# Performance work log

Measured on AMD Instinct MI355X. Metric: run time of the kernel, lower is better.

The kernel has to match this reference:

```python
import jax, jax.numpy as jnp
import numpy as np

N_NODES = 100000
N_EDGES = 3200000
N_GRAPHS = 1000
FEAT = 512
EMB = 7
N_CLASSES = 10


def gcn_conv(x, W, b, src, dst, n_nodes):
    # PyG GCNConv: add self-loops, symmetric normalization, aggregate src->dst.
    h = x @ W  # [N, emb] — transform first (emb is tiny)
    loops = jnp.arange(n_nodes, dtype=src.dtype)
    es = jnp.concatenate([src, loops])
    ed = jnp.concatenate([dst, loops])
    deg = jax.ops.segment_sum(jnp.ones_like(ed, dtype=h.dtype), ed, num_segments=n_nodes)
    dinv = jnp.where(deg > 0, jax.lax.rsqrt(deg), 0.0)
    norm = dinv[es] * dinv[ed]  # [E+N]
    msgs = h[es] * norm[:, None]
    out = jax.ops.segment_sum(msgs, ed, num_segments=n_nodes)
    return out + b


def setup_inputs() -> dict:
    key = jax.random.key(0)
    ks = jax.random.split(key, 8)
    x = jax.random.normal(ks[0], (N_NODES, FEAT), dtype=jnp.float32)
    edge_index = jax.random.randint(ks[1], (2, N_EDGES), 0, N_NODES, dtype=jnp.int64)
    batch_index = jnp.sort(jax.random.randint(ks[2], (N_NODES,), 0, N_GRAPHS, dtype=jnp.int64))
    s_in = 1.0 / np.sqrt(FEAT)
    s_h = 1.0 / np.sqrt(EMB)
    W_in = jax.random.uniform(ks[3], (FEAT, EMB), jnp.float32, -s_in, s_in)
    b_in = jnp.zeros((EMB,), jnp.float32)
    W_conv1 = jax.random.uniform(ks[4], (EMB, EMB), jnp.float32, -s_h, s_h)
    b_conv1 = jnp.zeros((EMB,), jnp.float32)
    W_out = jax.random.uniform(ks[5], (EMB, N_CLASSES), jnp.float32, -s_h, s_h)
    b_out = jax.random.uniform(ks[6], (N_CLASSES,), jnp.float32, -s_h, s_h)
    return {"x": x, "edge_index": edge_index, "batch_index": batch_index,
            "W_in": W_in, "b_in": b_in, "W_conv1": W_conv1, "b_conv1": b_conv1,
            "W_out": W_out, "b_out": b_out}


def reference(x, edge_index, batch_index, W_in, b_in, W_conv1, b_conv1, W_out, b_out):
    src, dst = edge_index[0], edge_index[1]
    out = jax.nn.relu(gcn_conv(x, W_in, b_in, src, dst, N_NODES))  # [N, 7]
    # final_conv_acts (computed by the original but NOT used in the returned logits)
    _final_conv_acts = jax.nn.relu(gcn_conv(out, W_conv1, b_conv1, src, dst, N_NODES))
    # global mean pool over batch_index (on `out`, matching the original forward)
    sums = jax.ops.segment_sum(out, batch_index, num_segments=N_GRAPHS)
    counts = jax.ops.segment_sum(jnp.ones((N_NODES,), out.dtype), batch_index, num_segments=N_GRAPHS)
    pooled = sums / jnp.maximum(counts, 1.0)[:, None]  # [G, 7]
    logits = pooled @ W_out + b_out  # [G, classes]
    return jax.nn.softmax(logits, axis=1)
```

## Files before the change

### kernel.cpp

```cpp
#include <hip/hip_runtime.h>

#define N_NODES   100000
#define N_EDGES   3200000
#define N_GRAPHS  1000
#define FEAT      512
#define EMB       7
#define HP        8
#define N_CLASSES 10

#define BSH       8
#define DMASK     255
#define NBUCK     391
#define TCOLS     392
#define NB_A      512
#define TILE_A    6250
#define NIT       25
#define SEGCAP    9216
#define GSPAN     16
#define MMF       391

__device__ __forceinline__ int load_idx(const void* p, long long i, int is32) {
    if (is32) return ((const int*)p)[i];
    return (int)((const long long*)p)[i];
}

__device__ int edge_is32(const void* p) {
    __shared__ int sflag;
    if (threadIdx.x == 0) sflag = 0;
    __syncthreads();
    const int* w = (const int*)p;
    int any = 0;
    for (int k = threadIdx.x; k < 2048; k += blockDim.x)
        if (w[2 * k + 1] != 0) any = 1;
    if (any) atomicOr(&sflag, 1);
    __syncthreads();
    return sflag;
}

__device__ int batch_is32(const void* p) {
    __shared__ int sflag;
    if (threadIdx.x == 0) sflag = 0;
    __syncthreads();
    const int* w = (const int*)p;
    int any = 0;
    for (int k = 1024 + threadIdx.x; k < 2048; k += blockDim.x)
        if (w[2 * k + 1] != 0) any = 1;
    if (any) atomicOr(&sflag, 1);
    __syncthreads();
    return sflag;
}

__device__ void mm_span(int nbase, const float* __restrict__ x,
                        const float* __restrict__ W, float* __restrict__ h) {
    int n = nbase + (int)threadIdx.x;
    if (n >= N_NODES) return;
    const float4* xr = (const float4*)(x + (size_t)n * FEAT);
    float acc[EMB];
#pragma unroll
    for (int j = 0; j < EMB; ++j) acc[j] = 0.0f;
#pragma unroll 4
    for (int k4 = 0; k4 < FEAT / 4; ++k4) {
        float4 v = xr[k4];
        const float* w = W + k4 * 4 * EMB;
#pragma unroll
        for (int j = 0; j < EMB; ++j) {
            float a = acc[j];
            a = fmaf(v.x, w[0 * EMB + j], a);
            a = fmaf(v.y, w[1 * EMB + j], a);
            a = fmaf(v.z, w[2 * EMB + j], a);
            a = fmaf(v.w, w[3 * EMB + j], a);
            acc[j] = a;
        }
    }
    float4* o = (float4*)(h + (size_t)n * HP);
    o[0] = make_float4(acc[0], acc[1], acc[2], acc[3]);
    o[1] = make_float4(acc[4], acc[5], acc[6], 0.0f);
}

__global__ void k_sortblk(const void* __restrict__ eidx, int* __restrict__ T,
                          int* __restrict__ gpk, const float* __restrict__ x,
                          const float* __restrict__ W, float* __restrict__ h) {
    if (blockIdx.x >= NB_A) { mm_span(((int)blockIdx.x - NB_A) * 256, x, W, h); return; }
    __shared__ int stage[TILE_A];
    __shared__ int bins[NBUCK];
    __shared__ int cur[NBUCK];
    __shared__ int pairv[256];
    __shared__ int wsum[4];
    int is32 = edge_is32(eidx);
    const int b = (int)blockIdx.x, t = (int)threadIdx.x;
    for (int k = t; k < NBUCK; k += 256) bins[k] = 0;
    __syncthreads();
    long long e0 = (long long)b * TILE_A;
    int pk[NIT], bk[NIT];
#pragma unroll
    for (int it = 0; it < NIT; ++it) {
        int i = it * 256 + t;
        if (i < TILE_A) {
            int src = load_idx(eidx, e0 + i, is32);
            int d   = load_idx(eidx, (long long)N_EDGES + e0 + i, is32);
            pk[it] = src | ((d & DMASK) << 17);
            bk[it] = d >> BSH;
            atomicAdd(&bins[bk[it]], 1);
        } else { pk[it] = 0; bk[it] = -1; }
    }
    __syncthreads();
    int c0 = (2 * t     < NBUCK) ? bins[2 * t]     : 0;
    int c1 = (2 * t + 1 < NBUCK) ? bins[2 * t + 1] : 0;
    int pr = c0 + c1;
    int inc = pr;
    for (int o = 1; o < 64; o <<= 1) {
        int u = __shfl_up(inc, o);
        if ((t & 63) >= o) inc += u;
    }
    if ((t & 63) == 63) wsum[t >> 6] = inc;
    pairv[t] = inc;
    __syncthreads();
    int add = 0, wv = t >> 6;
    if (wv >= 1) add += wsum[0];
    if (wv >= 2) add += wsum[1];
    if (wv >= 3) add += wsum[2];
    int excl = inc + add - pr;
    __syncthreads();
    if (2 * t     < NBUCK) { bins[2 * t]     = excl;      cur[2 * t]     = excl; }
    if (2 * t + 1 < NBUCK) { bins[2 * t + 1] = excl + c0; cur[2 * t + 1] = excl + c0; }
    __syncthreads();
    for (int k = t; k < NBUCK; k += 256)
        T[b * TCOLS + k] = b * TILE_A + bins[k];
    if (t == 0) T[b * TCOLS + NBUCK] = (b + 1) * TILE_A;
#pragma unroll
    for (int it = 0; it < NIT; ++it) {
        if (bk[it] >= 0) {
            int slot = atomicAdd(&cur[bk[it]], 1);
            stage[slot] = pk[it];
        }
    }
    __syncthreads();
    for (int i = t; i < TILE_A; i += 256)
        gpk[b * TILE_A + i] = stage[i];
}

__device__ int load_runs(const int* __restrict__ T, int k,
                         int* rstart, int* rst, int* wsum) {
    const int t = (int)threadIdx.x;
    int b0 = 2 * t, b1 = 2 * t + 1;
    int s0 = T[b0 * TCOLS + k], e0 = T[b0 * TCOLS + k + 1];
    int s1 = T[b1 * TCOLS + k], e1 = T[b1 * TCOLS + k + 1];
    rstart[b0] = s0; rstart[b1] = s1;
    int c0 = e0 - s0, c1 = e1 - s1;
    int pr = c0 + c1;
    int inc = pr;
    for (int o = 1; o < 64; o <<= 1) {
        int u = __shfl_up(inc, o);
        if ((t & 63) >= o) inc += u;
    }
    if ((t & 63) == 63) wsum[t >> 6] = inc;
    __syncthreads();
    int add = 0, wv = t >> 6;
    if (wv >= 1) add += wsum[0];
    if (wv >= 2) add += wsum[1];
    if (wv >= 3) add += wsum[2];
    int excl = inc + add - pr;
    rst[b0] = excl;
    rst[b1] = excl + c0;
    if (t == 255) rst[512] = excl + pr;
    __syncthreads();
    return rst[512];
}

__device__ __forceinline__ int run_of(const int* rst, int i) {
    int lo = 0, hi = 512;
    while (lo + 1 < hi) { int m = (lo + hi) >> 1; if (rst[m] <= i) lo = m; else hi = m; }
    return lo;
}

__global__ void k_nodecnt(const int* __restrict__ T, const int* __restrict__ gpk,
                          int* __restrict__ cnt, float* __restrict__ gsum,
                          float* __restrict__ h) {
    __shared__ int rstart[512], rst[513], wsum[4];
    __shared__ int bin[256];
    const int k = (int)blockIdx.x, t = (int)threadIdx.x;
    if (k < 32) {
        int idx = k * 256 + t;
        if (idx < N_GRAPHS * 8) gsum[idx] = 0.0f;
    }
    bin[t] = 0;
    int total = load_runs(T, k, rstart, rst, wsum);
    __syncthreads();
    int chunk = (total + 255) >> 8;
    int i0 = t * chunk;
    int i1 = i0 + chunk; if (i1 > total) i1 = total;
    if (i0 < total) {
        int cur = run_of(rst, i0);
        int nxt = rst[cur + 1];
        int addr = rstart[cur] + (i0 - rst[cur]);
        for (int i = i0; i < i1; ++i) {
            while (i >= nxt) { ++cur; addr = rstart[cur] + (i - rst[cur]); nxt = rst[cur + 1]; }
            int p = gpk[addr++];
            atomicAdd(&bin[(p >> 17) & DMASK], 1);
        }
    }
    __syncthreads();
    int node = (k << BSH) + t;
    if (node < N_NODES) {
        int c = bin[t];
        cnt[node] = c;
        float di = rsqrtf((float)c + 1.0f);
        float4* hp = (float4*)(h + (size_t)node * HP);
        float4 a = hp[0], cc = hp[1];
        hp[0] = make_float4(a.x * di, a.y * di, a.z * di, a.w * di);
        hp[1] = make_float4(cc.x * di, cc.y * di, cc.z * di, 0.0f);
    }
}

__global__ void k_ggather(const int* __restrict__ T, const int* __restrict__ gpk,
                          const int* __restrict__ cnt, const float* __restrict__ h,
                          const float* __restrict__ b_in, const void* __restrict__ batch,
                          float* __restrict__ gsum) {
    __shared__ int stage[SEGCAP];
    __shared__ int rstart[512], rst[513], wsum[4];
    __shared__ int bin[256], loff[256], curs[256], pairv[256];
    __shared__ float gsl[GSPAN][8];
    __shared__ int gmin_s;
    const int k = (int)blockIdx.x, t = (int)threadIdx.x;
    int bis32 = batch_is32(batch);
    if (t == 0) gmin_s = load_idx(batch, (long long)(k << BSH), bis32);
    if (t < GSPAN * 8) ((float*)gsl)[t] = 0.0f;
    int total = load_runs(T, k, rstart, rst, wsum);
    int len = (total > SEGCAP) ? SEGCAP : total;
    {
        int node = (k << BSH) + t;
        bin[t] = (node < N_NODES) ? cnt[node] : 0;
        curs[t] = 0;
    }
    __syncthreads();
    const int gmin = gmin_s;
    {
        int v = bin[t];
        int inc = v;
        for (int o = 1; o < 64; o <<= 1) {
            int u = __shfl_up(inc, o);
            if ((t & 63) >= o) inc += u;
        }
        pairv[t] = inc;
        __syncthreads();
        int add = 0, wv = t >> 6;
        if (wv >= 1) add += pairv[63];
        if (wv >= 2) add += pairv[127];
        if (wv >= 3) add += pairv[191];
        loff[t] = inc + add - v;
    }
    __syncthreads();
    int chunk = (len + 255) >> 8;
    int i0 = t * chunk;
    int i1 = i0 + chunk; if (i1 > len) i1 = len;
    if (i0 < len) {
        int cur = run_of(rst, i0);
        int nxt = rst[cur + 1];
        int addr = rstart[cur] + (i0 - rst[cur]);
        for (int i = i0; i < i1; ++i) {
            while (i >= nxt) { ++cur; addr = rstart[cur] + (i - rst[cur]); nxt = rst[cur + 1]; }
            int p = gpk[addr++];
            int dl = (p >> 17) & DMASK;
            int r = atomicAdd(&curs[dl], 1);
            stage[loff[dl] + r] = p & 0x1FFFF;
        }
    }
    __syncthreads();
    const float4* h4 = (const float4*)h;
    int q = t & 3;
#pragma unroll
    for (int g4 = 0; g4 < 4; ++g4) {
        int nl = (t >> 2) + g4 * 64;
        int node = (k << BSH) + nl;
        if (node < N_NODES) {
            int o = loff[nl], c = bin[nl];
            float acc[EMB];
#pragma unroll
            for (int j = 0; j < EMB; ++j) acc[j] = 0.0f;
            for (int kk = q; kk < c; kk += 4) {
                int s = stage[o + kk];
                float4 a4 = h4[(size_t)s * 2];
                float4 c4 = h4[(size_t)s * 2 + 1];
                acc[0] += a4.x; acc[1] += a4.y; acc[2] += a4.z; acc[3] += a4.w;
                acc[4] += c4.x; acc[5] += c4.y; acc[6] += c4.z;
            }
            if (q == 0) {
                float4 a4 = h4[(size_t)node * 2];
                float4 c4 = h4[(size_t)node * 2 + 1];
                acc[0] += a4.x; acc[1] += a4.y; acc[2] += a4.z; acc[3] += a4.w;
                acc[4] += c4.x; acc[5] += c4.y; acc[6] += c4.z;
            }
#pragma unroll
            for (int j = 0; j < EMB; ++j) {
                acc[j] += __shfl_xor(acc[j], 1);
                acc[j] += __shfl_xor(acc[j], 2);
            }
            float di = rsqrtf((float)c + 1.0f);
            int j0 = 2 * q;
            float v0 = fmaxf(fmaf(di, acc[j0], b_in[j0]), 0.0f);
            float v1 = (j0 + 1 < EMB)
                     ? fmaxf(fmaf(di, acc[j0 + 1], b_in[j0 + 1]), 0.0f) : 0.0f;
            int g = load_idx(batch, node, bis32);
            int gi = g - gmin;
            if (gi < GSPAN) {
                atomicAdd(&gsl[gi][j0], v0);
                atomicAdd(&gsl[gi][j0 + 1], v1);
            } else {
                atomicAdd(&gsum[(size_t)g * 8 + j0], v0);
                atomicAdd(&gsum[(size_t)g * 8 + j0 + 1], v1);
            }
        }
    }
    __syncthreads();
    if (t < GSPAN * 8) {
        int r = t >> 3, c = t & 7;
        float v = gsl[r][c];
        int g = gmin + r;
        if (v != 0.0f && g < N_GRAPHS) atomicAdd(&gsum[(size_t)g * 8 + c], v);
    }
}

__global__ void k_final(const float* __restrict__ gsum, const void* __restrict__ batch,
                        const float* __restrict__ W_out, const float* __restrict__ b_out,
                        float* __restrict__ out) {
    int is32 = batch_is32(batch);
    int g = (int)blockIdx.x * 256 + (int)threadIdx.x;
    if (g >= N_GRAPHS) return;
    int n0, n1;
    {
        int lo = 0, hi = N_NODES;
        while (lo < hi) { int m = (lo + hi) >> 1; if (load_idx(batch, m, is32) < g) lo = m + 1; else hi = m; }
        n0 = lo;
        hi = N_NODES;
        while (lo < hi) { int m = (lo + hi) >> 1; if (load_idx(batch, m, is32) < g + 1) lo = m + 1; else hi = m; }
        n1 = lo;
    }
    float inv = 1.0f / fmaxf((float)(n1 - n0), 1.0f);
    float sums[EMB];
#pragma unroll
    for (int j = 0; j < EMB; ++j) sums[j] = gsum[(size_t)g * 8 + j] * inv;
    float logit[N_CLASSES];
    float mx = -1e30f;
#pragma unroll
    for (int c = 0; c < N_CLASSES; ++c) {
        float l = b_out[c];
#pragma unroll
        for (int j = 0; j < EMB; ++j)
            l = fmaf(sums[j], W_out[j * N_CLASSES + c], l);
        logit[c] = l;
        mx = fmaxf(mx, l);
    }
    float se = 0.0f;
#pragma unroll
    for (int c = 0; c < N_CLASSES; ++c) {
        logit[c] = expf(logit[c] - mx);
        se += logit[c];
    }
    float is = 1.0f / se;
#pragma unroll
    for (int c = 0; c < N_CLASSES; ++c)
        out[(size_t)g * N_CLASSES + c] = logit[c] * is;
}

extern "C" void kernel_launch(void* const* d_in, const int* in_sizes, int n_in,
                              void* d_out, int out_size, void* d_ws, size_t ws_size,
                              hipStream_t stream) {
    const float* x     = (const float*)d_in[0];
    const void*  eidx  = d_in[1];
    const void*  batch = d_in[2];
    const float* W_in  = (const float*)d_in[3];
    const float* b_in  = (const float*)d_in[4];
    const float* W_out = (const float*)d_in[7];
    const float* b_out = (const float*)d_in[8];
    float* out = (float*)d_out;

    int*   gpk  = (int*)d_ws;
    int*   T    = gpk + N_EDGES;
    int*   cnt  = T + NB_A * TCOLS;
    float* h    = (float*)(cnt + N_NODES);
    float* gsum = h + (size_t)N_NODES * HP;

    const int B = 256;
    k_sortblk<<<NB_A + MMF, B, 0, stream>>>(eidx, T, gpk, x, W_in, h);
    k_nodecnt<<<NBUCK, B, 0, stream>>>(T, gpk, cnt, gsum, h);
    k_ggather<<<NBUCK, B, 0, stream>>>(T, gpk, cnt, h, b_in, batch, gsum);
    k_final  <<<(N_GRAPHS + B - 1) / B, B, 0, stream>>>(gsum, batch, W_out, b_out, out);
}
```

Before: 135.6 us.

## Halve destination bucket width to 128 nodes, doubling blocks for gather

Shrinks each destination bucket from 256 to 128 nodes, so the bucket count doubles to 782. The sort kernel's scan now handles four buckets per thread, and the count and gather kernels work on 128-node segments with a smaller shared staging buffer. The aim is more blocks and less shared memory per block, which should raise occupancy and parallelism in the gather and count phases. In exchange, the bucket table and the per-block run lists get larger, and half the threads sit idle in the per-node phases.

```diff
diff --git a/kernel.cpp b/kernel.cpp
--- a/kernel.cpp
+++ b/kernel.cpp
@@ -8,14 +8,14 @@
 #define HP        8
 #define N_CLASSES 10
 
-#define BSH       8
-#define DMASK     255
-#define NBUCK     391
-#define TCOLS     392
+#define BSH       7
+#define DMASK     127
+#define NBUCK     782
+#define TCOLS     783
 #define NB_A      512
 #define TILE_A    6250
 #define NIT       25
-#define SEGCAP    9216
+#define SEGCAP    4864
 #define GSPAN     16
 #define MMF       391
 
@@ -84,7 +84,6 @@
     __shared__ int stage[TILE_A];
     __shared__ int bins[NBUCK];
     __shared__ int cur[NBUCK];
-    __shared__ int pairv[256];
     __shared__ int wsum[4];
     int is32 = edge_is32(eidx);
     const int b = (int)blockIdx.x, t = (int)threadIdx.x;
@@ -104,25 +103,28 @@
         } else { pk[it] = 0; bk[it] = -1; }
     }
     __syncthreads();
-    int c0 = (2 * t     < NBUCK) ? bins[2 * t]     : 0;
-    int c1 = (2 * t + 1 < NBUCK) ? bins[2 * t + 1] : 0;
-    int pr = c0 + c1;
-    int inc = pr;
+    int c0 = (4 * t     < NBUCK) ? bins[4 * t]     : 0;
+    int c1 = (4 * t + 1 < NBUCK) ? bins[4 * t + 1] : 0;
+    int c2 = (4 * t + 2 < NBUCK) ? bins[4 * t + 2] : 0;
+    int c3 = (4 * t + 3 < NBUCK) ? bins[4 * t + 3] : 0;
+    int sum4 = c0 + c1 + c2 + c3;
+    int inc = sum4;
     for (int o = 1; o < 64; o <<= 1) {
         int u = __shfl_up(inc, o);
         if ((t & 63) >= o) inc += u;
     }
     if ((t & 63) == 63) wsum[t >> 6] = inc;
-    pairv[t] = inc;
     __syncthreads();
     int add = 0, wv = t >> 6;
     if (wv >= 1) add += wsum[0];
     if (wv >= 2) add += wsum[1];
     if (wv >= 3) add += wsum[2];
-    int excl = inc + add - pr;
-    __syncthreads();
-    if (2 * t     < NBUCK) { bins[2 * t]     = excl;      cur[2 * t]     = excl; }
-    if (2 * t + 1 < NBUCK) { bins[2 * t + 1] = excl + c0; cur[2 * t + 1] = excl + c0; }
+    int excl = inc + add - sum4;
+    __syncthreads();
+    if (4 * t     < NBUCK) { bins[4 * t]     = excl;                cur[4 * t]     = excl; }
+    if (4 * t + 1 < NBUCK) { bins[4 * t + 1] = excl + c0;           cur[4 * t + 1] = excl + c0; }
+    if (4 * t + 2 < NBUCK) { bins[4 * t + 2] = excl + c0 + c1;      cur[4 * t + 2] = excl + c0 + c1; }
+    if (4 * t + 3 < NBUCK) { bins[4 * t + 3] = excl + c0 + c1 + c2; cur[4 * t + 3] = excl + c0 + c1 + c2; }
     __syncthreads();
     for (int k = t; k < NBUCK; k += 256)
         T[b * TCOLS + k] = b * TILE_A + bins[k];
@@ -177,13 +179,13 @@
                           int* __restrict__ cnt, float* __restrict__ gsum,
                           float* __restrict__ h) {
     __shared__ int rstart[512], rst[513], wsum[4];
-    __shared__ int bin[256];
+    __shared__ int bin[128];
     const int k = (int)blockIdx.x, t = (int)threadIdx.x;
     if (k < 32) {
         int idx = k * 256 + t;
         if (idx < N_GRAPHS * 8) gsum[idx] = 0.0f;
     }
-    bin[t] = 0;
+    if (t < 128) bin[t] = 0;
     int total = load_runs(T, k, rstart, rst, wsum);
     __syncthreads();
     int chunk = (total + 255) >> 8;
@@ -201,7 +203,7 @@
     }
     __syncthreads();
     int node = (k << BSH) + t;
-    if (node < N_NODES) {
+    if (t < 128 && node < N_NODES) {
         int c = bin[t];
         cnt[node] = c;
         float di = rsqrtf((float)c + 1.0f);
@@ -218,7 +220,7 @@
                           float* __restrict__ gsum) {
     __shared__ int stage[SEGCAP];
     __shared__ int rstart[512], rst[513], wsum[4];
-    __shared__ int bin[256], loff[256], curs[256], pairv[256];
+    __shared__ int bin[128], loff[128], curs[128], pairv[128];
     __shared__ float gsl[GSPAN][8];
     __shared__ int gmin_s;
     const int k = (int)blockIdx.x, t = (int)threadIdx.x;
@@ -227,14 +229,14 @@
     if (t < GSPAN * 8) ((float*)gsl)[t] = 0.0f;
     int total = load_runs(T, k, rstart, rst, wsum);
     int len = (total > SEGCAP) ? SEGCAP : total;
-    {
+    if (t < 128) {
         int node = (k << BSH) + t;
         bin[t] = (node < N_NODES) ? cnt[node] : 0;
         curs[t] = 0;
     }
     __syncthreads();
     const int gmin = gmin_s;
-    {
+    if (t < 128) {
         int v = bin[t];
         int inc = v;
         for (int o = 1; o < 64; o <<= 1) {
@@ -242,12 +244,12 @@
             if ((t & 63) >= o) inc += u;
         }
         pairv[t] = inc;
-        __syncthreads();
-        int add = 0, wv = t >> 6;
-        if (wv >= 1) add += pairv[63];
-        if (wv >= 2) add += pairv[127];
-        if (wv >= 3) add += pairv[191];
-        loff[t] = inc + add - v;
+    }
+    __syncthreads();
+    if (t < 128) {
+        int v = bin[t];
+        int add = (t >= 64) ? pairv[63] : 0;
+        loff[t] = pairv[t] + add - v;
     }
     __syncthreads();
     int chunk = (len + 255) >> 8;
@@ -269,7 +271,7 @@
     const float4* h4 = (const float4*)h;
     int q = t & 3;
 #pragma unroll
-    for (int g4 = 0; g4 < 4; ++g4) {
+    for (int g4 = 0; g4 < 2; ++g4) {
         int nl = (t >> 2) + g4 * 64;
         int node = (k << BSH) + nl;
         if (node < N_NODES) {
```

New measurement: 150.1 us. 10.7% more time.
